# Optimization experiments

Hardware: AMD Instinct MI355X
Metric: run time of the kernel (lower is better)

## Reference

```python
import jax, jax.numpy as jnp
import numpy as np

B, S, D, H = 2, 2048, 1024, 16


def setup_inputs() -> dict:
    key = jax.random.key(0)
    kq, kk, kv1, kv2 = jax.random.split(key, 4)
    return {
        "q": jax.random.normal(kq, (B, S, D), dtype=jnp.float32),
        "k": jax.random.normal(kk, (B, S, D), dtype=jnp.float32),
        "v1": jax.random.normal(kv1, (B, S, D), dtype=jnp.float32),
        "v2": jax.random.normal(kv2, (B, S, D), dtype=jnp.float32),
        "num_attn_heads": 16,
    }


def _split_heads(x, h):
    b, s, d = x.shape
    return x.reshape(b, s, h, d // h).transpose(0, 2, 1, 3)  # [B,H,S,dh]


def reference(q, k, v1, v2, num_attn_heads):
    h = num_attn_heads
    b, s, d = q.shape
    dh = d // h
    qh = _split_heads(q, h)
    kh = _split_heads(k, h)
    v1h = _split_heads(v1, h)
    v2h = _split_heads(v2, h)
    scores = jnp.einsum("bhqd,bhkd->bhqk", qh, kh) / jnp.sqrt(jnp.float32(dh))
    # Faithful to create_mask(input, 0): nopeek = triu(ones, k=0); mask = (nopeek == 0)
    # -> only STRICTLY lower triangle is visible; diagonal and above get -1e9.
    # Row 0 is fully masked -> softmax uniform (same as torch behavior).
    allowed = jnp.tril(jnp.ones((s, s), dtype=bool), k=-1)  # [S,S] j < i
    scores = jnp.where(allowed[None, None], scores, jnp.float32(-1e9))
    p_attn = jax.nn.softmax(scores, axis=-1)  # dropout p=0.0 -> identity
    o1 = jnp.einsum("bhqk,bhkd->bhqd", p_attn, v1h)
    o2 = jnp.einsum("bhqk,bhkd->bhqd", p_attn, v2h)
    o1 = o1.transpose(0, 2, 1, 3).reshape(b, s, d)
    o2 = o2.transpose(0, 2, 1, 3).reshape(b, s, d)
    return (o1, o2)
```

## Files before the change

kernel.cpp:

```cpp
#include <hip/hip_runtime.h>

#define B_ 2
#define S_ 2048
#define D_ 1024
#define H_ 16
#define DH 64
#define OFF2 (B_ * S_ * D_)

typedef __attribute__((ext_vector_type(8))) __bf16 bf16x8;
typedef __attribute__((ext_vector_type(4))) float f32x4;
typedef __attribute__((ext_vector_type(4))) unsigned int u32x4;
typedef __attribute__((address_space(3))) unsigned int lds_u32;
typedef __attribute__((address_space(1))) const unsigned int glob_u32;

__device__ __forceinline__ unsigned short f2bf(float f) {
    return __builtin_bit_cast(unsigned short, (__bf16)f);
}
__device__ __forceinline__ float bf2f(unsigned short h) {
    unsigned int u = ((unsigned int)h) << 16;
    return __builtin_bit_cast(float, u);
}

template <int CTRL>
__device__ __forceinline__ float dpp_ror(float x) {
    return __builtin_bit_cast(float, __builtin_amdgcn_update_dpp(
        0, __builtin_bit_cast(int, x), CTRL, 0xf, 0xf, false));
}
__device__ __forceinline__ float rowsum16(float x) {
    x += dpp_ror<0x121>(x);
    x += dpp_ror<0x122>(x);
    x += dpp_ror<0x124>(x);
    x += dpp_ror<0x128>(x);
    return x;
}

__global__ void prep_all(const float* __restrict__ q, const float* __restrict__ k,
                         const float* __restrict__ v1, const float* __restrict__ v2,
                         unsigned short* __restrict__ qb, unsigned short* __restrict__ kb,
                         unsigned short* __restrict__ v1t, unsigned short* __restrict__ v2t) {
    int id = blockIdx.x;
    if (id < 4096) {
        int ysel = id & 1;
        int cid = (id >> 1) * 256 + threadIdx.x;
        const float* src = ysel ? k : q;
        unsigned short* dst = ysel ? kb : qb;
        float scale = ysel ? 1.0f : 0.125f * 1.4426950408889634f;
        int d8 = cid & 7;
        int s  = (cid >> 3) & (S_ - 1);
        int h  = (cid >> 14) & (H_ - 1);
        int b  = cid >> 18;
        int off = (b * S_ + s) * D_ + h * DH + d8 * 8;
        float4 f0 = *(const float4*)(src + off);
        float4 f1 = *(const float4*)(src + off + 4);
        unsigned int w0 = f2bf(f0.x * scale) | ((unsigned int)f2bf(f0.y * scale) << 16);
        unsigned int w1 = f2bf(f0.z * scale) | ((unsigned int)f2bf(f0.w * scale) << 16);
        unsigned int w2 = f2bf(f1.x * scale) | ((unsigned int)f2bf(f1.y * scale) << 16);
        unsigned int w3 = f2bf(f1.z * scale) | ((unsigned int)f2bf(f1.w * scale) << 16);
        u32x4 wv = {w0, w1, w2, w3};
        *(u32x4*)(dst + cid * 8) = wv;
        return;
    }
    __shared__ __align__(16) unsigned short ldsT[64][72];
    int id2 = id - 4096;
    int t = threadIdx.x;
    int s0 = (id2 & 31) * 64;
    int bh = (id2 >> 5) & 31;
    int b = bh >> 4, h = bh & 15;
    const float* src = (id2 >> 10) ? v2 : v1;
    unsigned short* dst = (id2 >> 10) ? v2t : v1t;
    {
        int sl = t >> 2, dc = t & 3;
        int off = (b * S_ + s0 + sl) * D_ + h * DH + dc * 16;
#pragma unroll
        for (int i4 = 0; i4 < 4; i4++) {
            float4 f = *(const float4*)(src + off + i4 * 4);
            int d = dc * 16 + i4 * 4;
            ldsT[d + 0][sl] = f2bf(f.x);
            ldsT[d + 1][sl] = f2bf(f.y);
            ldsT[d + 2][sl] = f2bf(f.z);
            ldsT[d + 3][sl] = f2bf(f.w);
        }
    }
    __syncthreads();
    {
        int d = t >> 2, sc = t & 3;
        u32x4 a = *(const u32x4*)(&ldsT[d][sc * 16]);
        u32x4 c = *(const u32x4*)(&ldsT[d][sc * 16 + 8]);
        int off = (bh * DH + d) * S_ + s0 + sc * 16;
        *(u32x4*)(dst + off) = a;
        *(u32x4*)(dst + off + 8) = c;
    }
}

__global__ __launch_bounds__(256) void flash_attn(
        const unsigned short* __restrict__ qb, const unsigned short* __restrict__ kb,
        const unsigned short* __restrict__ v1t, const unsigned short* __restrict__ v2t,
        float* __restrict__ out) {
    __shared__ __align__(16) unsigned short sK0[4096], sK1[4096];
    __shared__ __align__(16) unsigned short sV1[4096], sV2[4096];
    __shared__ __align__(16) unsigned short sP[4096];

    int tid = threadIdx.x;
    int w = tid >> 6, lane = tid & 63;
    int lr = lane & 15, lg = lane >> 4;

    int id = blockIdx.x;
    int xcd = id & 7;
    int j = id >> 3;
    int bh = xcd * 4 + (j & 3);
    int qt = 31 - (j >> 2);

    const unsigned short* gK  = kb  + bh * (S_ * DH);
    const unsigned short* gV1 = v1t + bh * (DH * S_);
    const unsigned short* gV2 = v2t + bh * (DH * S_);

    int srow = tid >> 3, sco = tid & 7;

    auto stageV = [&](int t) {
#pragma unroll
        for (int jj = 0; jj < 2; jj++) {
            int row = srow + jj * 32;
            int cosw = (sco ^ (row & 7)) * 8;
            int c8 = (tid + jj * 256) * 8;
            __builtin_amdgcn_global_load_lds((glob_u32*)(gV1 + row * S_ + t * 64 + cosw),
                                             (lds_u32*)(sV1 + c8), 16, 0, 0);
            __builtin_amdgcn_global_load_lds((glob_u32*)(gV2 + row * S_ + t * 64 + cosw),
                                             (lds_u32*)(sV2 + c8), 16, 0, 0);
        }
    };
    auto stageK = [&](unsigned short* dK, int t) {
#pragma unroll
        for (int jj = 0; jj < 2; jj++) {
            int row = srow + jj * 32;
            int cosw = (sco ^ (row & 7)) * 8;
            int c8 = (tid + jj * 256) * 8;
            __builtin_amdgcn_global_load_lds((glob_u32*)(gK + (t * 64 + row) * 64 + cosw),
                                             (lds_u32*)(dK + c8), 16, 0, 0);
        }
    };

    bf16x8 qa[2];
    {
        int qoff = (bh * S_ + qt * 64 + w * 16 + lr) * DH + lg * 8;
        qa[0] = __builtin_bit_cast(bf16x8, *(const u32x4*)(qb + qoff));
        qa[1] = __builtin_bit_cast(bf16x8, *(const u32x4*)(qb + qoff + 32));
    }

    int tz = w >> 1, half = w & 1;
    const unsigned short* cV = tz ? sV2 : sV1;

    f32x4 acc[2][4];
    float l[4];
#pragma unroll
    for (int m = 0; m < 2; m++)
#pragma unroll
        for (int dt = 0; dt < 4; dt++) acc[m][dt] = (f32x4){0.f, 0.f, 0.f, 0.f};
#pragma unroll
    for (int r = 0; r < 4; r++) l[r] = 0.f;

    stageK(sK0, 0);

    for (int t = 0; t <= qt; t++) {
        const unsigned short* cK = (t & 1) ? sK1 : sK0;
        unsigned short* nK       = (t & 1) ? sK0 : sK1;
        __builtin_amdgcn_s_barrier();
        stageV(t);
        stageK(nK, (t < qt) ? t + 1 : qt);
        asm volatile("s_waitcnt vmcnt(6)" ::: "memory");
        f32x4 s[4];
        __builtin_amdgcn_s_setprio(1);
#pragma unroll
        for (int n = 0; n < 4; n++) {
            f32x4 accs = (f32x4){0.f, 0.f, 0.f, 0.f};
#pragma unroll
            for (int ks = 0; ks < 2; ks++) {
                int kv = n * 16 + lr;
                int idx = ((kv << 6) + ks * 32 + lg * 8) ^ ((kv & 7) << 3);
                bf16x8 bk = __builtin_bit_cast(bf16x8, *(const u32x4*)(cK + idx));
                accs = __builtin_amdgcn_mfma_f32_16x16x32_bf16(qa[ks], bk, accs, 0, 0, 0);
            }
            s[n] = accs;
        }
        __builtin_amdgcn_s_setprio(0);
        if (t == qt) {
#pragma unroll
            for (int n = 0; n < 4; n++) {
                int kv = n * 16 + lr;
#pragma unroll
                for (int r = 0; r < 4; r++) {
                    int qrow = w * 16 + lg * 4 + r;
                    if (kv >= qrow) s[n][r] = -1e30f;
                }
            }
        }
#pragma unroll
        for (int n = 0; n < 4; n++)
#pragma unroll
            for (int r = 0; r < 4; r++) {
                float pv = __builtin_amdgcn_exp2f(s[n][r] - 20.0f);
                l[r] += pv;
                int row = w * 16 + lg * 4 + r, col = n * 16 + lr;
                sP[((row << 6) + col) ^ ((row & 7) << 3)] = f2bf(pv);
            }
        asm volatile("s_waitcnt lgkmcnt(0)" ::: "memory");
        asm volatile("s_waitcnt vmcnt(2)" ::: "memory");
        __builtin_amdgcn_s_barrier();
        __builtin_amdgcn_s_setprio(1);
#pragma unroll
        for (int ks = 0; ks < 2; ks++)
#pragma unroll
            for (int m = 0; m < 2; m++) {
                int row = half * 32 + m * 16 + lr;
                int pidx = ((row << 6) + ks * 32 + lg * 8) ^ ((row & 7) << 3);
                bf16x8 ap = __builtin_bit_cast(bf16x8, *(const u32x4*)(sP + pidx));
#pragma unroll
                for (int dt = 0; dt < 4; dt++) {
                    int d = dt * 16 + lr;
                    int vidx = ((d << 6) + ks * 32 + lg * 8) ^ ((d & 7) << 3);
                    bf16x8 bv = __builtin_bit_cast(bf16x8, *(const u32x4*)(cV + vidx));
                    acc[m][dt] = __builtin_amdgcn_mfma_f32_16x16x32_bf16(ap, bv, acc[m][dt], 0, 0, 0);
                }
            }
        __builtin_amdgcn_s_setprio(0);
    }

    asm volatile("s_waitcnt vmcnt(0)" ::: "memory");
    __builtin_amdgcn_s_barrier();
    float* lsh = (float*)sK0;
#pragma unroll
    for (int r = 0; r < 4; r++) {
        float ls = rowsum16(l[r]);
        if (lr == 0) lsh[w * 16 + lg * 4 + r] = ls;
    }
    asm volatile("s_waitcnt lgkmcnt(0)" ::: "memory");
    __builtin_amdgcn_s_barrier();

    {
        int b = bh >> 4, h = bh & 15;
#pragma unroll
        for (int m = 0; m < 2; m++)
#pragma unroll
            for (int r = 0; r < 4; r++) {
                int row = half * 32 + m * 16 + lg * 4 + r;
                float inv = 1.0f / lsh[row];
                int qrow = qt * 64 + row;
                int base = (b * S_ + qrow) * D_ + h * DH + lr + tz * OFF2;
#pragma unroll
                for (int dt = 0; dt < 4; dt++)
                    out[base + dt * 16] = acc[m][dt][r] * inv;
            }
    }
}

__global__ void row0_mean(const unsigned short* __restrict__ v1t,
                          const unsigned short* __restrict__ v2t,
                          float* __restrict__ out) {
    int wid = blockIdx.x * 4 + (threadIdx.x >> 6);
    int lane = threadIdx.x & 63;
    int tz = wid >> 11;
    int bhd = wid & 2047;
    const unsigned short* src = (tz ? v2t : v1t) + bhd * S_;
    float sum = 0.f;
#pragma unroll
    for (int kk = 0; kk < 4; kk++) {
        u32x4 v = *(const u32x4*)(src + (kk * 64 + lane) * 8);
#pragma unroll
        for (int jj = 0; jj < 4; jj++) {
            unsigned int u = v[jj];
            sum += bf2f((unsigned short)(u & 0xffff)) + bf2f((unsigned short)(u >> 16));
        }
    }
#pragma unroll
    for (int msk = 32; msk >= 1; msk >>= 1) sum += __shfl_xor(sum, msk, 64);
    if (lane == 0) {
        int b = bhd >> 10, rem = bhd & 1023, h = rem >> 6, d = rem & 63;
        out[tz * OFF2 + b * (S_ * D_) + h * DH + d] = sum * (1.0f / S_);
    }
}

extern "C" void kernel_launch(void* const* d_in, const int* in_sizes, int n_in,
                              void* d_out, int out_size, void* d_ws, size_t ws_size,
                              hipStream_t stream) {
    const float* q  = (const float*)d_in[0];
    const float* k  = (const float*)d_in[1];
    const float* v1 = (const float*)d_in[2];
    const float* v2 = (const float*)d_in[3];
    float* out = (float*)d_out;

    const int ELEMS = B_ * H_ * S_ * DH;
    unsigned short* qb  = (unsigned short*)d_ws;
    unsigned short* kb  = qb + ELEMS;
    unsigned short* v1t = kb + ELEMS;
    unsigned short* v2t = v1t + ELEMS;

    prep_all<<<6144, 256, 0, stream>>>(q, k, v1, v2, qb, kb, v1t, v2t);
    flash_attn<<<1024, 256, 0, stream>>>(qb, kb, v1t, v2t, out);
    row0_mean<<<1024, 256, 0, stream>>>(v1t, v2t, out);
}
```

Baseline: 74.23 us.

## Double query tile to 128 rows per block to reuse K/V tiles

Each block now handles 128 query rows instead of 64, with each wave computing two 16-row Q fragments, so every staged K and V tile in LDS feeds twice as many MFMAs. The grid is halved to 512 blocks and the P buffer doubled. This cuts global K/V traffic and staging overhead per unit of work. In exchange it raises register pressure (larger accumulators), increases LDS use, and leaves fewer blocks for load balancing across CUs under the causal workload.

Result: slower. 87.42 us (+17.8%).

```diff
diff --git a/kernel.cpp b/kernel.cpp
--- a/kernel.cpp
+++ b/kernel.cpp
@@ -98,7 +98,7 @@
         float* __restrict__ out) {
     __shared__ __align__(16) unsigned short sK0[4096], sK1[4096];
     __shared__ __align__(16) unsigned short sV1[4096], sV2[4096];
-    __shared__ __align__(16) unsigned short sP[4096];
+    __shared__ __align__(16) unsigned short sP[8192];
 
     int tid = threadIdx.x;
     int w = tid >> 6, lane = tid & 63;
@@ -108,7 +108,9 @@
     int xcd = id & 7;
     int j = id >> 3;
     int bh = xcd * 4 + (j & 3);
-    int qt = 31 - (j >> 2);
+    int qt = 15 - (j >> 2);
+    int nt = 2 * qt + 2;
+    int q0 = qt * 128;
 
     const unsigned short* gK  = kb  + bh * (S_ * DH);
     const unsigned short* gV1 = v1t + bh * (DH * S_);
@@ -139,88 +141,102 @@
         }
     };
 
-    bf16x8 qa[2];
-    {
-        int qoff = (bh * S_ + qt * 64 + w * 16 + lr) * DH + lg * 8;
-        qa[0] = __builtin_bit_cast(bf16x8, *(const u32x4*)(qb + qoff));
-        qa[1] = __builtin_bit_cast(bf16x8, *(const u32x4*)(qb + qoff + 32));
+    bf16x8 qa[2][2];
+#pragma unroll
+    for (int m = 0; m < 2; m++) {
+        int qoff = (bh * S_ + q0 + w * 32 + m * 16 + lr) * DH + lg * 8;
+        qa[m][0] = __builtin_bit_cast(bf16x8, *(const u32x4*)(qb + qoff));
+        qa[m][1] = __builtin_bit_cast(bf16x8, *(const u32x4*)(qb + qoff + 32));
     }
 
     int tz = w >> 1, half = w & 1;
     const unsigned short* cV = tz ? sV2 : sV1;
 
-    f32x4 acc[2][4];
-    float l[4];
+    f32x4 acc[4][4];
+    float l[2][4];
+#pragma unroll
+    for (int mp = 0; mp < 4; mp++)
+#pragma unroll
+        for (int dt = 0; dt < 4; dt++) acc[mp][dt] = (f32x4){0.f, 0.f, 0.f, 0.f};
 #pragma unroll
     for (int m = 0; m < 2; m++)
 #pragma unroll
-        for (int dt = 0; dt < 4; dt++) acc[m][dt] = (f32x4){0.f, 0.f, 0.f, 0.f};
-#pragma unroll
-    for (int r = 0; r < 4; r++) l[r] = 0.f;
+        for (int r = 0; r < 4; r++) l[m][r] = 0.f;
 
     stageK(sK0, 0);
 
-    for (int t = 0; t <= qt; t++) {
+    for (int t = 0; t < nt; t++) {
         const unsigned short* cK = (t & 1) ? sK1 : sK0;
         unsigned short* nK       = (t & 1) ? sK0 : sK1;
         __builtin_amdgcn_s_barrier();
         stageV(t);
-        stageK(nK, (t < qt) ? t + 1 : qt);
+        stageK(nK, (t < nt - 1) ? t + 1 : t);
         asm volatile("s_waitcnt vmcnt(6)" ::: "memory");
-        f32x4 s[4];
+        f32x4 s[2][4];
         __builtin_amdgcn_s_setprio(1);
 #pragma unroll
         for (int n = 0; n < 4; n++) {
-            f32x4 accs = (f32x4){0.f, 0.f, 0.f, 0.f};
-#pragma unroll
-            for (int ks = 0; ks < 2; ks++) {
-                int kv = n * 16 + lr;
-                int idx = ((kv << 6) + ks * 32 + lg * 8) ^ ((kv & 7) << 3);
-                bf16x8 bk = __builtin_bit_cast(bf16x8, *(const u32x4*)(cK + idx));
-                accs = __builtin_amdgcn_mfma_f32_16x16x32_bf16(qa[ks], bk, accs, 0, 0, 0);
-            }
-            s[n] = accs;
+            int kv = n * 16 + lr;
+            int i0 = ((kv << 6) + lg * 8) ^ ((kv & 7) << 3);
+            bf16x8 k0 = __builtin_bit_cast(bf16x8, *(const u32x4*)(cK + i0));
+            bf16x8 k1 = __builtin_bit_cast(bf16x8, *(const u32x4*)(cK + (i0 ^ 32)));
+#pragma unroll
+            for (int m = 0; m < 2; m++) {
+                f32x4 a = __builtin_amdgcn_mfma_f32_16x16x32_bf16(
+                    qa[m][0], k0, (f32x4){0.f, 0.f, 0.f, 0.f}, 0, 0, 0);
+                s[m][n] = __builtin_amdgcn_mfma_f32_16x16x32_bf16(qa[m][1], k1, a, 0, 0, 0);
+            }
         }
         __builtin_amdgcn_s_setprio(0);
-        if (t == qt) {
+        if (t >= 2 * qt) {
 #pragma unroll
             for (int n = 0; n < 4; n++) {
-                int kv = n * 16 + lr;
+                int kvg = t * 64 + n * 16 + lr;
+#pragma unroll
+                for (int m = 0; m < 2; m++) {
+#pragma unroll
+                    for (int r = 0; r < 4; r++) {
+                        int qg = q0 + w * 32 + m * 16 + lg * 4 + r;
+                        if (kvg >= qg) s[m][n][r] = -1e30f;
+                    }
+                }
+            }
+        }
+#pragma unroll
+        for (int m = 0; m < 2; m++)
+#pragma unroll
+            for (int n = 0; n < 4; n++)
 #pragma unroll
                 for (int r = 0; r < 4; r++) {
-                    int qrow = w * 16 + lg * 4 + r;
-                    if (kv >= qrow) s[n][r] = -1e30f;
+                    float pv = __builtin_amdgcn_exp2f(s[m][n][r] - 20.0f);
+                    l[m][r] += pv;
+                    int row = w * 32 + m * 16 + lg * 4 + r, col = n * 16 + lr;
+                    sP[((row << 6) + col) ^ ((row & 7) << 3)] = f2bf(pv);
                 }
-            }
-        }
-#pragma unroll
-        for (int n = 0; n < 4; n++)
-#pragma unroll
-            for (int r = 0; r < 4; r++) {
-                float pv = __builtin_amdgcn_exp2f(s[n][r] - 20.0f);
-                l[r] += pv;
-                int row = w * 16 + lg * 4 + r, col = n * 16 + lr;
-                sP[((row << 6) + col) ^ ((row & 7) << 3)] = f2bf(pv);
-            }
         asm volatile("s_waitcnt lgkmcnt(0)" ::: "memory");
         asm volatile("s_waitcnt vmcnt(2)" ::: "memory");
         __builtin_amdgcn_s_barrier();
         __builtin_amdgcn_s_setprio(1);
 #pragma unroll
-        for (int ks = 0; ks < 2; ks++)
-#pragma unroll
-            for (int m = 0; m < 2; m++) {
-                int row = half * 32 + m * 16 + lr;
-                int pidx = ((row << 6) + ks * 32 + lg * 8) ^ ((row & 7) << 3);
-                bf16x8 ap = __builtin_bit_cast(bf16x8, *(const u32x4*)(sP + pidx));
-#pragma unroll
-                for (int dt = 0; dt < 4; dt++) {
-                    int d = dt * 16 + lr;
-                    int vidx = ((d << 6) + ks * 32 + lg * 8) ^ ((d & 7) << 3);
-                    bf16x8 bv = __builtin_bit_cast(bf16x8, *(const u32x4*)(cV + vidx));
-                    acc[m][dt] = __builtin_amdgcn_mfma_f32_16x16x32_bf16(ap, bv, acc[m][dt], 0, 0, 0);
-                }
-            }
+        for (int ks = 0; ks < 2; ks++) {
+            bf16x8 pf[4];
+#pragma unroll
+            for (int mp = 0; mp < 4; mp++) {
+                int row = half * 64 + mp * 16 + lr;
+                pf[mp] = __builtin_bit_cast(bf16x8, *(const u32x4*)(
+                    sP + (((row << 6) + ks * 32 + lg * 8) ^ ((row & 7) << 3))));
+            }
+#pragma unroll
+            for (int dt = 0; dt < 4; dt++) {
+                int d = dt * 16 + lr;
+                bf16x8 vf = __builtin_bit_cast(bf16x8, *(const u32x4*)(
+                    cV + (((d << 6) + ks * 32 + lg * 8) ^ ((d & 7) << 3))));
+#pragma unroll
+                for (int mp = 0; mp < 4; mp++)
+                    acc[mp][dt] = __builtin_amdgcn_mfma_f32_16x16x32_bf16(
+                        pf[mp], vf, acc[mp][dt], 0, 0, 0);
+            }
+        }
         __builtin_amdgcn_s_setprio(0);
     }
 
@@ -228,26 +244,27 @@
     __builtin_amdgcn_s_barrier();
     float* lsh = (float*)sK0;
 #pragma unroll
-    for (int r = 0; r < 4; r++) {
-        float ls = rowsum16(l[r]);
-        if (lr == 0) lsh[w * 16 + lg * 4 + r] = ls;
-    }
+    for (int m = 0; m < 2; m++)
+#pragma unroll
+        for (int r = 0; r < 4; r++) {
+            float ls = rowsum16(l[m][r]);
+            if (lr == 0) lsh[w * 32 + m * 16 + lg * 4 + r] = ls;
+        }
     asm volatile("s_waitcnt lgkmcnt(0)" ::: "memory");
     __builtin_amdgcn_s_barrier();
 
     {
         int b = bh >> 4, h = bh & 15;
 #pragma unroll
-        for (int m = 0; m < 2; m++)
+        for (int mp = 0; mp < 4; mp++)
 #pragma unroll
             for (int r = 0; r < 4; r++) {
-                int row = half * 32 + m * 16 + lg * 4 + r;
+                int row = half * 64 + mp * 16 + lg * 4 + r;
                 float inv = 1.0f / lsh[row];
-                int qrow = qt * 64 + row;
-                int base = (b * S_ + qrow) * D_ + h * DH + lr + tz * OFF2;
+                int base = (b * S_ + q0 + row) * D_ + h * DH + lr + tz * OFF2;
 #pragma unroll
                 for (int dt = 0; dt < 4; dt++)
-                    out[base + dt * 16] = acc[m][dt][r] * inv;
+                    out[base + dt * 16] = acc[mp][dt][r] * inv;
             }
     }
 }
@@ -294,6 +311,6 @@
     unsigned short* v2t = v1t + ELEMS;
 
     prep_all<<<6144, 256, 0, stream>>>(q, k, v1, v2, qb, kb, v1t, v2t);
-    flash_attn<<<1024, 256, 0, stream>>>(qb, kb, v1t, v2t, out);
+    flash_attn<<<512, 256, 0, stream>>>(qb, kb, v1t, v2t, out);
     row0_mean<<<1024, 256, 0, stream>>>(v1t, v2t, out);
 }
```

## Load-balance causal attention by pairing q-tiles, fuse Q/K conversion into attention

Applied to the files above, without the earlier changes.

Each block now processes a pair of query tiles (31-p and p), splitting the long tile's work across two blocks. Partial results are accumulated with atomics into a zeroed output, and a separate normalize kernel divides by atomically summed row denominators. Q and K are read as fp32 straight from the input and converted to bf16 in registers, so the bf16 prep pass for Q/K is gone and the K buffer is single-buffered. The exp offset is folded into the MFMA accumulator init. In exchange it adds memsets, fp32 atomics, an extra normalize pass, and more fp32 global traffic for K, which is re-read by many blocks.

Result: slower. 119.7 us (+61.3%).

```diff
diff --git a/kernel.cpp b/kernel.cpp
--- a/kernel.cpp
+++ b/kernel.cpp
@@ -6,6 +6,7 @@
 #define H_ 16
 #define DH 64
 #define OFF2 (B_ * S_ * D_)
+#define ELEMS (B_ * H_ * S_ * DH)
 
 typedef __attribute__((ext_vector_type(8))) __bf16 bf16x8;
 typedef __attribute__((ext_vector_type(4))) float f32x4;
@@ -15,6 +16,9 @@
 
 __device__ __forceinline__ unsigned short f2bf(float f) {
     return __builtin_bit_cast(unsigned short, (__bf16)f);
+}
+__device__ __forceinline__ unsigned int pk2(float a, float b) {
+    return (unsigned int)f2bf(a) | ((unsigned int)f2bf(b) << 16);
 }
 __device__ __forceinline__ float bf2f(unsigned short h) {
     unsigned int u = ((unsigned int)h) << 16;
@@ -34,40 +38,16 @@
     return x;
 }
 
-__global__ void prep_all(const float* __restrict__ q, const float* __restrict__ k,
-                         const float* __restrict__ v1, const float* __restrict__ v2,
-                         unsigned short* __restrict__ qb, unsigned short* __restrict__ kb,
-                         unsigned short* __restrict__ v1t, unsigned short* __restrict__ v2t) {
+__global__ void prep_v(const float* __restrict__ v1, const float* __restrict__ v2,
+                       unsigned short* __restrict__ v1t, unsigned short* __restrict__ v2t) {
+    __shared__ __align__(16) unsigned short ldsT[64][72];
     int id = blockIdx.x;
-    if (id < 4096) {
-        int ysel = id & 1;
-        int cid = (id >> 1) * 256 + threadIdx.x;
-        const float* src = ysel ? k : q;
-        unsigned short* dst = ysel ? kb : qb;
-        float scale = ysel ? 1.0f : 0.125f * 1.4426950408889634f;
-        int d8 = cid & 7;
-        int s  = (cid >> 3) & (S_ - 1);
-        int h  = (cid >> 14) & (H_ - 1);
-        int b  = cid >> 18;
-        int off = (b * S_ + s) * D_ + h * DH + d8 * 8;
-        float4 f0 = *(const float4*)(src + off);
-        float4 f1 = *(const float4*)(src + off + 4);
-        unsigned int w0 = f2bf(f0.x * scale) | ((unsigned int)f2bf(f0.y * scale) << 16);
-        unsigned int w1 = f2bf(f0.z * scale) | ((unsigned int)f2bf(f0.w * scale) << 16);
-        unsigned int w2 = f2bf(f1.x * scale) | ((unsigned int)f2bf(f1.y * scale) << 16);
-        unsigned int w3 = f2bf(f1.z * scale) | ((unsigned int)f2bf(f1.w * scale) << 16);
-        u32x4 wv = {w0, w1, w2, w3};
-        *(u32x4*)(dst + cid * 8) = wv;
-        return;
-    }
-    __shared__ __align__(16) unsigned short ldsT[64][72];
-    int id2 = id - 4096;
     int t = threadIdx.x;
-    int s0 = (id2 & 31) * 64;
-    int bh = (id2 >> 5) & 31;
+    int s0 = (id & 31) * 64;
+    int bh = (id >> 5) & 31;
     int b = bh >> 4, h = bh & 15;
-    const float* src = (id2 >> 10) ? v2 : v1;
-    unsigned short* dst = (id2 >> 10) ? v2t : v1t;
+    const float* src = (id >> 10) ? v2 : v1;
+    unsigned short* dst = (id >> 10) ? v2t : v1t;
     {
         int sl = t >> 2, dc = t & 3;
         int off = (b * S_ + s0 + sl) * D_ + h * DH + dc * 16;
@@ -93,28 +73,30 @@
 }
 
 __global__ __launch_bounds__(256) void flash_attn(
-        const unsigned short* __restrict__ qb, const unsigned short* __restrict__ kb,
+        const float* __restrict__ qf, const float* __restrict__ kf,
         const unsigned short* __restrict__ v1t, const unsigned short* __restrict__ v2t,
-        float* __restrict__ out) {
-    __shared__ __align__(16) unsigned short sK0[4096], sK1[4096];
+        float* __restrict__ out, float* __restrict__ lws) {
+    __shared__ __align__(16) unsigned short sK[4096];
     __shared__ __align__(16) unsigned short sV1[4096], sV2[4096];
     __shared__ __align__(16) unsigned short sP[4096];
 
     int tid = threadIdx.x;
     int w = tid >> 6, lane = tid & 63;
     int lr = lane & 15, lg = lane >> 4;
+    int srow = tid >> 3, sco = tid & 7;
 
     int id = blockIdx.x;
-    int xcd = id & 7;
-    int j = id >> 3;
-    int bh = xcd * 4 + (j & 3);
-    int qt = 31 - (j >> 2);
-
-    const unsigned short* gK  = kb  + bh * (S_ * DH);
+    int bh = (id & 7) * 4 + ((id >> 3) & 3);
+    int rest = id >> 5;
+    int p = rest & 15, h = rest >> 4;
+    int qA = 31 - p, qB = p;
+    int i0 = h ? 17 : 0, i1 = h ? 32 : 16;
+    int b = bh >> 4, hh = bh & 15;
+
     const unsigned short* gV1 = v1t + bh * (DH * S_);
     const unsigned short* gV2 = v2t + bh * (DH * S_);
-
-    int srow = tid >> 3, sco = tid & 7;
+    const float* gKf = kf + (size_t)b * S_ * D_ + hh * DH;
+    const float qscale = 0.125f * 1.4426950408889634f;
 
     auto stageV = [&](int t) {
 #pragma unroll
@@ -128,61 +110,97 @@
                                              (lds_u32*)(sV2 + c8), 16, 0, 0);
         }
     };
-    auto stageK = [&](unsigned short* dK, int t) {
-#pragma unroll
-        for (int jj = 0; jj < 2; jj++) {
-            int row = srow + jj * 32;
-            int cosw = (sco ^ (row & 7)) * 8;
-            int c8 = (tid + jj * 256) * 8;
-            __builtin_amdgcn_global_load_lds((glob_u32*)(gK + (t * 64 + row) * 64 + cosw),
-                                             (lds_u32*)(dK + c8), 16, 0, 0);
-        }
-    };
-
+
+    float4 kr0, kr1, kr2, kr3;
+    auto issueK = [&](int t) {
+        int rowa = srow, rowb = srow + 32;
+        const float* pa = gKf + (t * 64 + rowa) * D_ + (sco ^ (rowa & 7)) * 8;
+        const float* pb = gKf + (t * 64 + rowb) * D_ + (sco ^ (rowb & 7)) * 8;
+        kr0 = *(const float4*)pa; kr1 = *(const float4*)(pa + 4);
+        kr2 = *(const float4*)pb; kr3 = *(const float4*)(pb + 4);
+    };
+    auto writeK = [&]() {
+        u32x4 w0 = {pk2(kr0.x, kr0.y), pk2(kr0.z, kr0.w), pk2(kr1.x, kr1.y), pk2(kr1.z, kr1.w)};
+        u32x4 w1 = {pk2(kr2.x, kr2.y), pk2(kr2.z, kr2.w), pk2(kr3.x, kr3.y), pk2(kr3.z, kr3.w)};
+        *(u32x4*)(sK + tid * 8) = w0;
+        *(u32x4*)(sK + (tid + 256) * 8) = w1;
+    };
+
+    float4 qr0, qr1, qr2, qr3;
     bf16x8 qa[2];
-    {
-        int qoff = (bh * S_ + qt * 64 + w * 16 + lr) * DH + lg * 8;
-        qa[0] = __builtin_bit_cast(bf16x8, *(const u32x4*)(qb + qoff));
-        qa[1] = __builtin_bit_cast(bf16x8, *(const u32x4*)(qb + qoff + 32));
-    }
+    auto issueQ = [&](int qt) {
+        const float* a = qf + ((size_t)b * S_ + qt * 64 + w * 16 + lr) * D_ + hh * DH + lg * 8;
+        qr0 = *(const float4*)a; qr1 = *(const float4*)(a + 4);
+        qr2 = *(const float4*)(a + 32); qr3 = *(const float4*)(a + 36);
+    };
+    auto cvtQ = [&]() {
+        u32x4 w0 = {pk2(qr0.x * qscale, qr0.y * qscale), pk2(qr0.z * qscale, qr0.w * qscale),
+                    pk2(qr1.x * qscale, qr1.y * qscale), pk2(qr1.z * qscale, qr1.w * qscale)};
+        u32x4 w1 = {pk2(qr2.x * qscale, qr2.y * qscale), pk2(qr2.z * qscale, qr2.w * qscale),
+                    pk2(qr3.x * qscale, qr3.y * qscale), pk2(qr3.z * qscale, qr3.w * qscale)};
+        qa[0] = __builtin_bit_cast(bf16x8, w0);
+        qa[1] = __builtin_bit_cast(bf16x8, w1);
+    };
 
     int tz = w >> 1, half = w & 1;
     const unsigned short* cV = tz ? sV2 : sV1;
 
     f32x4 acc[2][4];
     float l[4];
-#pragma unroll
-    for (int m = 0; m < 2; m++)
-#pragma unroll
-        for (int dt = 0; dt < 4; dt++) acc[m][dt] = (f32x4){0.f, 0.f, 0.f, 0.f};
-#pragma unroll
-    for (int r = 0; r < 4; r++) l[r] = 0.f;
-
-    stageK(sK0, 0);
-
-    for (int t = 0; t <= qt; t++) {
-        const unsigned short* cK = (t & 1) ? sK1 : sK0;
-        unsigned short* nK       = (t & 1) ? sK0 : sK1;
+    auto initState = [&]() {
+#pragma unroll
+        for (int m = 0; m < 2; m++)
+#pragma unroll
+            for (int dt = 0; dt < 4; dt++) acc[m][dt] = (f32x4){0.f, 0.f, 0.f, 0.f};
+#pragma unroll
+        for (int r = 0; r < 4; r++) l[r] = 0.f;
+    };
+    auto partialAtomic = [&](int qt) {
+#pragma unroll
+        for (int m = 0; m < 2; m++)
+#pragma unroll
+            for (int dt = 0; dt < 4; dt++)
+#pragma unroll
+                for (int r = 0; r < 4; r++) {
+                    int row = half * 32 + m * 16 + lg * 4 + r;
+                    int idx = tz * OFF2 + (b * S_ + qt * 64 + row) * D_ + hh * DH + dt * 16 + lr;
+                    atomicAdd(&out[idx], acc[m][dt][r]);
+                }
+#pragma unroll
+        for (int r = 0; r < 4; r++) {
+            float ls = rowsum16(l[r]);
+            if (lr == 0) atomicAdd(&lws[(bh * 16 + p) * 64 + w * 16 + lg * 4 + r], ls);
+        }
+    };
+
+    int qcur = h ? (qA >= 17 ? qA : qB) : qA;
+    initState();
+    issueQ(qcur);
+    issueK((i0 <= qA) ? i0 : i0 - qA - 1);
+    cvtQ();
+    writeK();
+
+    for (int i = i0; i <= i1; ++i) {
+        int kvt = (i <= qA) ? i : i - qA - 1;
+        asm volatile("s_waitcnt lgkmcnt(0)" ::: "memory");
         __builtin_amdgcn_s_barrier();
-        stageV(t);
-        stageK(nK, (t < qt) ? t + 1 : qt);
-        asm volatile("s_waitcnt vmcnt(6)" ::: "memory");
+        stageV(kvt);
+        int inx = (i < i1) ? i + 1 : i1;
+        issueK((inx <= qA) ? inx : inx - qA - 1);
         f32x4 s[4];
         __builtin_amdgcn_s_setprio(1);
 #pragma unroll
         for (int n = 0; n < 4; n++) {
-            f32x4 accs = (f32x4){0.f, 0.f, 0.f, 0.f};
-#pragma unroll
-            for (int ks = 0; ks < 2; ks++) {
-                int kv = n * 16 + lr;
-                int idx = ((kv << 6) + ks * 32 + lg * 8) ^ ((kv & 7) << 3);
-                bf16x8 bk = __builtin_bit_cast(bf16x8, *(const u32x4*)(cK + idx));
-                accs = __builtin_amdgcn_mfma_f32_16x16x32_bf16(qa[ks], bk, accs, 0, 0, 0);
-            }
-            s[n] = accs;
+            int kv = n * 16 + lr;
+            int ix = ((kv << 6) + lg * 8) ^ ((kv & 7) << 3);
+            bf16x8 k0 = __builtin_bit_cast(bf16x8, *(const u32x4*)(sK + ix));
+            bf16x8 k1 = __builtin_bit_cast(bf16x8, *(const u32x4*)(sK + (ix ^ 32)));
+            f32x4 a = __builtin_amdgcn_mfma_f32_16x16x32_bf16(
+                qa[0], k0, (f32x4){-20.f, -20.f, -20.f, -20.f}, 0, 0, 0);
+            s[n] = __builtin_amdgcn_mfma_f32_16x16x32_bf16(qa[1], k1, a, 0, 0, 0);
         }
         __builtin_amdgcn_s_setprio(0);
-        if (t == qt) {
+        if (i == qA || i == 32) {
 #pragma unroll
             for (int n = 0; n < 4; n++) {
                 int kv = n * 16 + lr;
@@ -197,58 +215,89 @@
         for (int n = 0; n < 4; n++)
 #pragma unroll
             for (int r = 0; r < 4; r++) {
-                float pv = __builtin_amdgcn_exp2f(s[n][r] - 20.0f);
+                float pv = __builtin_amdgcn_exp2f(s[n][r]);
                 l[r] += pv;
                 int row = w * 16 + lg * 4 + r, col = n * 16 + lr;
                 sP[((row << 6) + col) ^ ((row & 7) << 3)] = f2bf(pv);
             }
         asm volatile("s_waitcnt lgkmcnt(0)" ::: "memory");
-        asm volatile("s_waitcnt vmcnt(2)" ::: "memory");
+        asm volatile("s_waitcnt vmcnt(4)" ::: "memory");
         __builtin_amdgcn_s_barrier();
         __builtin_amdgcn_s_setprio(1);
 #pragma unroll
-        for (int ks = 0; ks < 2; ks++)
+        for (int ks = 0; ks < 2; ks++) {
+            bf16x8 pf[2];
 #pragma unroll
             for (int m = 0; m < 2; m++) {
                 int row = half * 32 + m * 16 + lr;
-                int pidx = ((row << 6) + ks * 32 + lg * 8) ^ ((row & 7) << 3);
-                bf16x8 ap = __builtin_bit_cast(bf16x8, *(const u32x4*)(sP + pidx));
-#pragma unroll
-                for (int dt = 0; dt < 4; dt++) {
-                    int d = dt * 16 + lr;
-                    int vidx = ((d << 6) + ks * 32 + lg * 8) ^ ((d & 7) << 3);
-                    bf16x8 bv = __builtin_bit_cast(bf16x8, *(const u32x4*)(cV + vidx));
-                    acc[m][dt] = __builtin_amdgcn_mfma_f32_16x16x32_bf16(ap, bv, acc[m][dt], 0, 0, 0);
-                }
-            }
+                pf[m] = __builtin_bit_cast(bf16x8, *(const u32x4*)(
+                    sP + (((row << 6) + ks * 32 + lg * 8) ^ ((row & 7) << 3))));
+            }
+#pragma unroll
+            for (int dt = 0; dt < 4; dt++) {
+                int d = dt * 16 + lr;
+                bf16x8 vf = __builtin_bit_cast(bf16x8, *(const u32x4*)(
+                    cV + (((d << 6) + ks * 32 + lg * 8) ^ ((d & 7) << 3))));
+#pragma unroll
+                for (int m = 0; m < 2; m++)
+                    acc[m][dt] = __builtin_amdgcn_mfma_f32_16x16x32_bf16(
+                        pf[m], vf, acc[m][dt], 0, 0, 0);
+            }
+        }
         __builtin_amdgcn_s_setprio(0);
-    }
-
-    asm volatile("s_waitcnt vmcnt(0)" ::: "memory");
-    __builtin_amdgcn_s_barrier();
-    float* lsh = (float*)sK0;
-#pragma unroll
-    for (int r = 0; r < 4; r++) {
-        float ls = rowsum16(l[r]);
-        if (lr == 0) lsh[w * 16 + lg * 4 + r] = ls;
-    }
+        if (i == qA && i < i1) {
+            issueQ(qB);
+            writeK();
+            partialAtomic(qA);
+            initState();
+            cvtQ();
+            qcur = qB;
+        } else {
+            writeK();
+        }
+    }
+
     asm volatile("s_waitcnt lgkmcnt(0)" ::: "memory");
     __builtin_amdgcn_s_barrier();
 
-    {
-        int b = bh >> 4, h = bh & 15;
+    if (h == 0) {
+        partialAtomic(qA);
+    } else {
+        float* lsh = (float*)sP;
+#pragma unroll
+        for (int r = 0; r < 4; r++) {
+            float ls = rowsum16(l[r]);
+            if (lr == 0) lsh[w * 16 + lg * 4 + r] = ls;
+        }
+        asm volatile("s_waitcnt lgkmcnt(0)" ::: "memory");
+        __builtin_amdgcn_s_barrier();
 #pragma unroll
         for (int m = 0; m < 2; m++)
 #pragma unroll
             for (int r = 0; r < 4; r++) {
                 int row = half * 32 + m * 16 + lg * 4 + r;
                 float inv = 1.0f / lsh[row];
-                int qrow = qt * 64 + row;
-                int base = (b * S_ + qrow) * D_ + h * DH + lr + tz * OFF2;
+                int base = tz * OFF2 + (b * S_ + qB * 64 + row) * D_ + hh * DH + lr;
 #pragma unroll
                 for (int dt = 0; dt < 4; dt++)
                     out[base + dt * 16] = acc[m][dt][r] * inv;
             }
+    }
+}
+
+__global__ void normalize_qA(float* __restrict__ out, const float* __restrict__ lws) {
+    int id = blockIdx.x;
+    int bh = id & 31, p = id >> 5;
+    int qA = 31 - p;
+    int b = bh >> 4, hh = bh & 15;
+    const float* lrow = lws + (bh * 16 + p) * 64;
+    int tid = threadIdx.x;
+#pragma unroll
+    for (int e = 0; e < 32; e++) {
+        int f = e * 256 + tid;
+        int tz = f >> 12, row = (f >> 6) & 63, d = f & 63;
+        int idx = tz * OFF2 + (b * S_ + qA * 64 + row) * D_ + hh * DH + d;
+        out[idx] = out[idx] / lrow[row];
     }
 }
 
@@ -287,13 +336,18 @@
     const float* v2 = (const float*)d_in[3];
     float* out = (float*)d_out;
 
-    const int ELEMS = B_ * H_ * S_ * DH;
-    unsigned short* qb  = (unsigned short*)d_ws;
-    unsigned short* kb  = qb + ELEMS;
-    unsigned short* v1t = kb + ELEMS;
+    unsigned short* v1t = (unsigned short*)d_ws;
     unsigned short* v2t = v1t + ELEMS;
-
-    prep_all<<<6144, 256, 0, stream>>>(q, k, v1, v2, qb, kb, v1t, v2t);
-    flash_attn<<<1024, 256, 0, stream>>>(qb, kb, v1t, v2t, out);
+    float* lws = (float*)(v2t + ELEMS);
+
+    hipMemsetAsync(lws, 0, 512 * 64 * sizeof(float), stream);
+    for (int tz = 0; tz < 2; tz++)
+        for (int b = 0; b < 2; b++)
+            hipMemsetAsync(out + tz * OFF2 + b * S_ * D_ + 1024 * D_, 0,
+                           (size_t)1024 * D_ * sizeof(float), stream);
+
+    prep_v<<<2048, 256, 0, stream>>>(v1, v2, v1t, v2t);
+    flash_attn<<<1024, 256, 0, stream>>>(q, k, v1t, v2t, out, lws);
+    normalize_qA<<<512, 256, 0, stream>>>(out, lws);
     row0_mean<<<1024, 256, 0, stream>>>(v1t, v2t, out);
 }
```

## Pair causal query tiles per block to balance work across blocks

Applied to the files above, without the earlier changes.

Each block now handles 32 query rows from tile 31-p and then from tile p, walking 33 KV tiles in one loop, so every block does the same amount of work. Within the QK step the four waves split the keys in halves instead of the rows, and the two partial row sums are combined in LDS at each epilogue. The -20 softmax offset is folded into the MFMA accumulator's starting value. In exchange, each block loads full K/V tiles while doing half the MFMA work per tile, which raises total K/V traffic. Reusing sP for row sums mid-loop may also race with other waves still reading P.

After: 78.49 us. +5.7%, slower.

```diff
diff --git a/kernel.cpp b/kernel.cpp
--- a/kernel.cpp
+++ b/kernel.cpp
@@ -6,6 +6,7 @@
 #define H_ 16
 #define DH 64
 #define OFF2 (B_ * S_ * D_)
+#define ELEMS (B_ * H_ * S_ * DH)
 
 typedef __attribute__((ext_vector_type(8))) __bf16 bf16x8;
 typedef __attribute__((ext_vector_type(4))) float f32x4;
@@ -98,23 +99,25 @@
         float* __restrict__ out) {
     __shared__ __align__(16) unsigned short sK0[4096], sK1[4096];
     __shared__ __align__(16) unsigned short sV1[4096], sV2[4096];
-    __shared__ __align__(16) unsigned short sP[4096];
+    __shared__ __align__(16) unsigned short sP[2048];
 
     int tid = threadIdx.x;
     int w = tid >> 6, lane = tid & 63;
     int lr = lane & 15, lg = lane >> 4;
+    int srow = tid >> 3, sco = tid & 7;
 
     int id = blockIdx.x;
-    int xcd = id & 7;
-    int j = id >> 3;
-    int bh = xcd * 4 + (j & 3);
-    int qt = 31 - (j >> 2);
+    int bh = (id & 7) * 4 + ((id >> 3) & 3);
+    int rest = id >> 5;
+    int p = rest & 15, rowhalf = rest >> 4;
+    int qA = 31 - p, qB = p;
+    int b = bh >> 4, hh = bh & 15;
+
+    int rg = (w & 1) * 16, kg = (w >> 1) * 32, tz = w >> 1;
 
     const unsigned short* gK  = kb  + bh * (S_ * DH);
     const unsigned short* gV1 = v1t + bh * (DH * S_);
     const unsigned short* gV2 = v2t + bh * (DH * S_);
-
-    int srow = tid >> 3, sco = tid & 7;
 
     auto stageV = [&](int t) {
 #pragma unroll
@@ -140,66 +143,87 @@
     };
 
     bf16x8 qa[2];
-    {
-        int qoff = (bh * S_ + qt * 64 + w * 16 + lr) * DH + lg * 8;
+    auto loadQ = [&](int qt) {
+        int qoff = (bh * S_ + qt * 64 + rowhalf * 32 + rg + lr) * DH + lg * 8;
         qa[0] = __builtin_bit_cast(bf16x8, *(const u32x4*)(qb + qoff));
         qa[1] = __builtin_bit_cast(bf16x8, *(const u32x4*)(qb + qoff + 32));
-    }
-
-    int tz = w >> 1, half = w & 1;
+    };
+
     const unsigned short* cV = tz ? sV2 : sV1;
 
-    f32x4 acc[2][4];
+    f32x4 acc[4];
     float l[4];
-#pragma unroll
-    for (int m = 0; m < 2; m++)
-#pragma unroll
-        for (int dt = 0; dt < 4; dt++) acc[m][dt] = (f32x4){0.f, 0.f, 0.f, 0.f};
-#pragma unroll
-    for (int r = 0; r < 4; r++) l[r] = 0.f;
-
+    auto initState = [&]() {
+#pragma unroll
+        for (int dt = 0; dt < 4; dt++) acc[dt] = (f32x4){0.f, 0.f, 0.f, 0.f};
+#pragma unroll
+        for (int r = 0; r < 4; r++) l[r] = 0.f;
+    };
+    auto epilogue = [&](int qt) {
+        float* lsh = (float*)sP;
+#pragma unroll
+        for (int r = 0; r < 4; r++) {
+            float ls = rowsum16(l[r]);
+            if (lr == 0) lsh[tz * 32 + rg + lg * 4 + r] = ls;
+        }
+        asm volatile("s_waitcnt lgkmcnt(0)" ::: "memory");
+        __builtin_amdgcn_s_barrier();
+#pragma unroll
+        for (int r = 0; r < 4; r++) {
+            int rowl = rg + lg * 4 + r;
+            float inv = 1.0f / (lsh[rowl] + lsh[32 + rowl]);
+            int base = tz * OFF2 + (b * S_ + qt * 64 + rowhalf * 32 + rowl) * D_ + hh * DH + lr;
+#pragma unroll
+            for (int dt = 0; dt < 4; dt++)
+                out[base + dt * 16] = acc[dt][r] * inv;
+        }
+    };
+
+    loadQ(qA);
+    initState();
     stageK(sK0, 0);
 
-    for (int t = 0; t <= qt; t++) {
-        const unsigned short* cK = (t & 1) ? sK1 : sK0;
-        unsigned short* nK       = (t & 1) ? sK0 : sK1;
+    for (int i = 0; i <= 32; i++) {
+        const unsigned short* cK = (i & 1) ? sK1 : sK0;
+        unsigned short* nK       = (i & 1) ? sK0 : sK1;
+        int kvt = (i <= qA) ? i : i - qA - 1;
         __builtin_amdgcn_s_barrier();
-        stageV(t);
-        stageK(nK, (t < qt) ? t + 1 : qt);
+        stageV(kvt);
+        int inx = (i < 32) ? i + 1 : 32;
+        stageK(nK, (inx <= qA) ? inx : inx - qA - 1);
         asm volatile("s_waitcnt vmcnt(6)" ::: "memory");
-        f32x4 s[4];
+        f32x4 s[2];
         __builtin_amdgcn_s_setprio(1);
 #pragma unroll
-        for (int n = 0; n < 4; n++) {
-            f32x4 accs = (f32x4){0.f, 0.f, 0.f, 0.f};
-#pragma unroll
-            for (int ks = 0; ks < 2; ks++) {
-                int kv = n * 16 + lr;
-                int idx = ((kv << 6) + ks * 32 + lg * 8) ^ ((kv & 7) << 3);
-                bf16x8 bk = __builtin_bit_cast(bf16x8, *(const u32x4*)(cK + idx));
-                accs = __builtin_amdgcn_mfma_f32_16x16x32_bf16(qa[ks], bk, accs, 0, 0, 0);
-            }
-            s[n] = accs;
+        for (int n = 0; n < 2; n++) {
+            int kv = kg + n * 16 + lr;
+            int ix0 = ((kv << 6) + lg * 8) ^ ((kv & 7) << 3);
+            int ix1 = ((kv << 6) + 32 + lg * 8) ^ ((kv & 7) << 3);
+            bf16x8 k0 = __builtin_bit_cast(bf16x8, *(const u32x4*)(cK + ix0));
+            bf16x8 k1 = __builtin_bit_cast(bf16x8, *(const u32x4*)(cK + ix1));
+            f32x4 a = __builtin_amdgcn_mfma_f32_16x16x32_bf16(
+                qa[0], k0, (f32x4){-20.f, -20.f, -20.f, -20.f}, 0, 0, 0);
+            s[n] = __builtin_amdgcn_mfma_f32_16x16x32_bf16(qa[1], k1, a, 0, 0, 0);
         }
         __builtin_amdgcn_s_setprio(0);
-        if (t == qt) {
-#pragma unroll
-            for (int n = 0; n < 4; n++) {
-                int kv = n * 16 + lr;
+        if (i == qA || i == 32) {
+#pragma unroll
+            for (int n = 0; n < 2; n++) {
+                int kv = kg + n * 16 + lr;
 #pragma unroll
                 for (int r = 0; r < 4; r++) {
-                    int qrow = w * 16 + lg * 4 + r;
+                    int qrow = rowhalf * 32 + rg + lg * 4 + r;
                     if (kv >= qrow) s[n][r] = -1e30f;
                 }
             }
         }
 #pragma unroll
-        for (int n = 0; n < 4; n++)
+        for (int n = 0; n < 2; n++)
 #pragma unroll
             for (int r = 0; r < 4; r++) {
-                float pv = __builtin_amdgcn_exp2f(s[n][r] - 20.0f);
+                float pv = __builtin_amdgcn_exp2f(s[n][r]);
                 l[r] += pv;
-                int row = w * 16 + lg * 4 + r, col = n * 16 + lr;
+                int row = rg + lg * 4 + r, col = kg + n * 16 + lr;
                 sP[((row << 6) + col) ^ ((row & 7) << 3)] = f2bf(pv);
             }
         asm volatile("s_waitcnt lgkmcnt(0)" ::: "memory");
@@ -207,49 +231,26 @@
         __builtin_amdgcn_s_barrier();
         __builtin_amdgcn_s_setprio(1);
 #pragma unroll
-        for (int ks = 0; ks < 2; ks++)
-#pragma unroll
-            for (int m = 0; m < 2; m++) {
-                int row = half * 32 + m * 16 + lr;
-                int pidx = ((row << 6) + ks * 32 + lg * 8) ^ ((row & 7) << 3);
-                bf16x8 ap = __builtin_bit_cast(bf16x8, *(const u32x4*)(sP + pidx));
-#pragma unroll
-                for (int dt = 0; dt < 4; dt++) {
-                    int d = dt * 16 + lr;
-                    int vidx = ((d << 6) + ks * 32 + lg * 8) ^ ((d & 7) << 3);
-                    bf16x8 bv = __builtin_bit_cast(bf16x8, *(const u32x4*)(cV + vidx));
-                    acc[m][dt] = __builtin_amdgcn_mfma_f32_16x16x32_bf16(ap, bv, acc[m][dt], 0, 0, 0);
-                }
+        for (int ks = 0; ks < 2; ks++) {
+            int prow = rg + lr;
+            bf16x8 pf = __builtin_bit_cast(bf16x8, *(const u32x4*)(
+                sP + (((prow << 6) + ks * 32 + lg * 8) ^ ((prow & 7) << 3))));
+#pragma unroll
+            for (int dt = 0; dt < 4; dt++) {
+                int d = dt * 16 + lr;
+                bf16x8 vf = __builtin_bit_cast(bf16x8, *(const u32x4*)(
+                    cV + (((d << 6) + ks * 32 + lg * 8) ^ ((d & 7) << 3))));
+                acc[dt] = __builtin_amdgcn_mfma_f32_16x16x32_bf16(pf, vf, acc[dt], 0, 0, 0);
             }
+        }
         __builtin_amdgcn_s_setprio(0);
-    }
-
-    asm volatile("s_waitcnt vmcnt(0)" ::: "memory");
-    __builtin_amdgcn_s_barrier();
-    float* lsh = (float*)sK0;
-#pragma unroll
-    for (int r = 0; r < 4; r++) {
-        float ls = rowsum16(l[r]);
-        if (lr == 0) lsh[w * 16 + lg * 4 + r] = ls;
-    }
-    asm volatile("s_waitcnt lgkmcnt(0)" ::: "memory");
-    __builtin_amdgcn_s_barrier();
-
-    {
-        int b = bh >> 4, h = bh & 15;
-#pragma unroll
-        for (int m = 0; m < 2; m++)
-#pragma unroll
-            for (int r = 0; r < 4; r++) {
-                int row = half * 32 + m * 16 + lg * 4 + r;
-                float inv = 1.0f / lsh[row];
-                int qrow = qt * 64 + row;
-                int base = (b * S_ + qrow) * D_ + h * DH + lr + tz * OFF2;
-#pragma unroll
-                for (int dt = 0; dt < 4; dt++)
-                    out[base + dt * 16] = acc[m][dt][r] * inv;
-            }
-    }
+        if (i == qA && i < 32) {
+            epilogue(qA);
+            initState();
+            loadQ(qB);
+        }
+    }
+    epilogue(qB);
 }
 
 __global__ void row0_mean(const unsigned short* __restrict__ v1t,
@@ -287,7 +288,6 @@
     const float* v2 = (const float*)d_in[3];
     float* out = (float*)d_out;
 
-    const int ELEMS = B_ * H_ * S_ * DH;
     unsigned short* qb  = (unsigned short*)d_ws;
     unsigned short* kb  = qb + ELEMS;
     unsigned short* v1t = kb + ELEMS;
```
